# Kernel optimization log

Hardware: AMD Instinct MI355X
Metric: run time of the kernel (lower is better)

## Reference

```python
import jax, jax.numpy as jnp
import numpy as np

C = 256
DR = 32  # C // reduction

def setup_inputs() -> dict:
    key = jax.random.key(0)
    ks = jax.random.split(key, 8)
    B, H, W = 8, 64, 64
    x = jax.random.normal(ks[0], (B, C, H, W), dtype=jnp.float32)
    # 1x1 conv weights stored as [out, in] matrices + biases
    sq = 1.0 / np.sqrt(C)
    Wq = jax.random.uniform(ks[1], (DR, C), minval=-sq, maxval=sq, dtype=jnp.float32)
    bq = jax.random.uniform(ks[2], (DR,), minval=-sq, maxval=sq, dtype=jnp.float32)
    Wk = jax.random.uniform(ks[3], (DR, C), minval=-sq, maxval=sq, dtype=jnp.float32)
    bk = jax.random.uniform(ks[4], (DR,), minval=-sq, maxval=sq, dtype=jnp.float32)
    Wv = jax.random.uniform(ks[5], (C, C), minval=-sq, maxval=sq, dtype=jnp.float32)
    bv = jax.random.uniform(ks[6], (C,), minval=-sq, maxval=sq, dtype=jnp.float32)
    gamma = jnp.zeros((1,), dtype=jnp.float32) + 0.5  # nonzero so output depends on attention
    return {"x": x, "Wq": Wq, "bq": bq, "Wk": Wk, "bk": bk, "Wv": Wv, "bv": bv, "gamma": gamma}

def reference(x, Wq, bq, Wk, bk, Wv, bv, gamma):
    B, Cc, H, W = x.shape
    N = H * W
    xf = x.reshape(B, Cc, N)                                   # [B,C,N]
    q = jnp.einsum('dc,bcn->bdn', Wq, xf) + bq[None, :, None]  # [B,DR,N]
    k = jnp.einsum('dc,bcn->bdn', Wk, xf) + bk[None, :, None]  # [B,DR,N]
    v = jnp.einsum('ec,bcn->ben', Wv, xf) + bv[None, :, None]  # [B,C,N]
    attn = jnp.einsum('bdi,bdj->bij', q, k)                    # [B,N,N]
    attn = jax.nn.softmax(attn, axis=-1)
    out = jnp.einsum('bcj,bij->bci', v, attn)                  # [B,C,N]
    out = out.reshape(B, Cc, H, W)
    return gamma * out + x
```

## Files before the change

### kernel.cpp

```cpp
#include <hip/hip_runtime.h>

#define LOG2E 1.44269504088896340736f

typedef short v8s __attribute__((ext_vector_type(8)));
typedef float v4f __attribute__((ext_vector_type(4)));
typedef unsigned int v2u __attribute__((ext_vector_type(2)));

__device__ __forceinline__ unsigned short f2bf(float f) {
  unsigned int u = __float_as_uint(f);
  u += 0x7fffu + ((u >> 16) & 1u);
  return (unsigned short)(u >> 16);
}

__device__ __forceinline__ unsigned int cvtpk(float lo, float hi) {
  unsigned int r;
  asm("v_cvt_pk_bf16_f32 %0, %1, %2" : "=v"(r) : "v"(lo), "v"(hi));
  return r;
}

#define MFMA16(a, b, c) __builtin_amdgcn_mfma_f32_16x16x32_bf16((a), (b), (c), 0, 0, 0)

static const int CCH = 256, NPIX = 4096;

__global__ void wconv_kernel(const float* __restrict__ Wq, const float* __restrict__ Wk,
                             const float* __restrict__ Wv, unsigned short* __restrict__ wqk,
                             unsigned short* __restrict__ wvb) {
  int idx = blockIdx.x * 256 + threadIdx.x;
  int tot = 64 * 256 + 256 * 256;
  for (int i = idx; i < tot; i += gridDim.x * 256) {
    if (i < 64 * 256) {
      float v = (i < 32 * 256) ? Wq[i] : Wk[i - 32 * 256];
      wqk[i] = f2bf(v);
    } else {
      wvb[i - 64 * 256] = f2bf(Wv[i - 64 * 256]);
    }
  }
}

__global__ void xpose_kernel(const float* __restrict__ x, unsigned short* __restrict__ xT) {
  __shared__ float tile[64][65];
  int bid = blockIdx.x;
  int b = bid >> 8;
  int c0 = ((bid >> 6) & 3) * 64;
  int n0 = (bid & 63) * 64;
  int t = threadIdx.x;
  const float* xp = x + ((size_t)b * CCH + c0) * NPIX + n0;
#pragma unroll
  for (int p = 0; p < 16; ++p) {
    int cc = p * 4 + (t >> 6);
    int nn = t & 63;
    tile[cc][nn] = xp[(size_t)cc * NPIX + nn];
  }
  __syncthreads();
  unsigned short* xo = xT + ((size_t)b * NPIX + n0) * CCH + c0;
#pragma unroll
  for (int p = 0; p < 8; ++p) {
    int nn = p * 8 + (t >> 5);
    int cc = (t & 31) * 2;
    unsigned int pk = (unsigned int)f2bf(tile[cc][nn]) |
                      ((unsigned int)f2bf(tile[cc + 1][nn]) << 16);
    *(unsigned int*)(xo + (size_t)nn * CCH + cc) = pk;
  }
}

__global__ __launch_bounds__(256, 2) void qkproj_kernel(
    const unsigned short* __restrict__ xT, const unsigned short* __restrict__ wqk,
    const float* __restrict__ bq, const float* __restrict__ bk,
    unsigned short* __restrict__ qb, unsigned short* __restrict__ kb) {
  int bid = blockIdx.x;
  int b = bid >> 6;
  int n0 = (bid & 63) * 64;
  int w = threadIdx.x >> 6, lane = threadIdx.x & 63, g = lane >> 4, li = lane & 15;
  int nrow = n0 + 16 * w;
  v4f acc[4];
#pragma unroll
  for (int dt = 0; dt < 4; ++dt) acc[dt] = (v4f){0.f, 0.f, 0.f, 0.f};
#pragma unroll
  for (int ks = 0; ks < 8; ++ks) {
    v8s a = *(const v8s*)(xT + ((size_t)(b * NPIX + nrow + li)) * CCH + ks * 32 + g * 8);
#pragma unroll
    for (int dt = 0; dt < 4; ++dt) {
      v8s bf = *(const v8s*)(wqk + (dt * 16 + li) * 256 + ks * 32 + g * 8);
      acc[dt] = MFMA16(a, bf, acc[dt]);
    }
  }
#pragma unroll
  for (int dt = 0; dt < 4; ++dt) {
    int d = (dt & 1) * 16 + li;
    float bias = (dt < 2) ? bq[d] : bk[d];
    unsigned short* op = (dt < 2) ? qb : kb;
#pragma unroll
    for (int r = 0; r < 4; ++r) {
      int n = nrow + 4 * g + r;
      op[((size_t)(b * NPIX + n)) * 32 + d] = f2bf(acc[dt][r] + bias);
    }
  }
}

__global__ __launch_bounds__(256, 2) void vproj_kernel(
    const unsigned short* __restrict__ xT, const unsigned short* __restrict__ wvb,
    const float* __restrict__ bv, unsigned short* __restrict__ vb) {
  int bid = blockIdx.x;
  int b = bid >> 6;
  int n0 = (bid & 63) * 64;
  int w = threadIdx.x >> 6, lane = threadIdx.x & 63, g = lane >> 4, li = lane & 15;
  v4f acc[4][4];
#pragma unroll
  for (int ct = 0; ct < 4; ++ct)
#pragma unroll
    for (int nt = 0; nt < 4; ++nt) acc[ct][nt] = (v4f){0.f, 0.f, 0.f, 0.f};
#pragma unroll
  for (int ks = 0; ks < 8; ++ks) {
    v8s xf[4];
#pragma unroll
    for (int nt = 0; nt < 4; ++nt)
      xf[nt] = *(const v8s*)(xT + ((size_t)(b * NPIX + n0 + nt * 16 + li)) * CCH + ks * 32 + g * 8);
#pragma unroll
    for (int ct = 0; ct < 4; ++ct) {
      v8s wf = *(const v8s*)(wvb + (w * 64 + ct * 16 + li) * 256 + ks * 32 + g * 8);
#pragma unroll
      for (int nt = 0; nt < 4; ++nt) acc[ct][nt] = MFMA16(wf, xf[nt], acc[ct][nt]);
    }
  }
#pragma unroll
  for (int ct = 0; ct < 4; ++ct)
#pragma unroll
    for (int r = 0; r < 4; ++r) {
      int c = w * 64 + ct * 16 + 4 * g + r;
      float bias = bv[c];
#pragma unroll
      for (int nt = 0; nt < 4; ++nt) {
        int n = n0 + nt * 16 + li;
        vb[((size_t)(b * CCH + c)) * NPIX + n] = f2bf(acc[ct][nt][r] + bias);
      }
    }
}

#define PSWZ(il, jl) (((il) * 64 + (jl)) ^ (((il) & 7) << 3))
__global__ __launch_bounds__(256, 2) void attn_kernel(
    const unsigned short* __restrict__ qb, const unsigned short* __restrict__ kb,
    const unsigned short* __restrict__ vb, const float* __restrict__ x,
    const float* __restrict__ gamma, float* __restrict__ out) {
  __shared__ __align__(16) unsigned short pbuf[2][64 * 64];
  __shared__ float fbuf[2][64];
  __shared__ float lbuf[64];
  int bx = blockIdx.x;
  int wg = (bx & 7) * 64 + (bx >> 3);
  int b = wg >> 6, it = wg & 63;
  int i0 = it * 64;
  int w = threadIdx.x >> 6, lane = threadIdx.x & 63, g = lane >> 4, li = lane & 15;

  v8s qf = *(const v8s*)(qb + ((size_t)(b * NPIX + i0 + w * 16 + li)) * 32 + g * 8);
  float mraw = -1e30f, ml2 = -1.44e30f, ls = 0.f;
  v4f acc[4][4];
#pragma unroll
  for (int ct = 0; ct < 4; ++ct)
#pragma unroll
    for (int itl = 0; itl < 4; ++itl) acc[ct][itl] = (v4f){0.f, 0.f, 0.f, 0.f};
  const v4f vzero = {0.f, 0.f, 0.f, 0.f};

  const unsigned short* kbase = kb + ((size_t)b * NPIX + li) * 32 + g * 8;
  const unsigned short* vb0 = vb + ((size_t)(b * CCH + w * 64 + li)) * NPIX + g * 8;
  const unsigned short* vbc[4];
#pragma unroll
  for (int ct = 0; ct < 4; ++ct) vbc[ct] = vb0 + (size_t)ct * 16 * NPIX;

  v8s kf[4];
#pragma unroll
  for (int jt = 0; jt < 4; ++jt) kf[jt] = *(const v8s*)(kbase + (size_t)(jt * 16) * 32);

  for (int jc = 0; jc < 64; ++jc) {
    int j0 = jc * 64, bsel = jc & 1;
    v4f s[4];
#pragma unroll
    for (int jt = 0; jt < 4; ++jt) s[jt] = MFMA16(kf[jt], qf, vzero);
    int jn = (jc < 63) ? j0 + 64 : j0;
#pragma unroll
    for (int jt = 0; jt < 4; ++jt)
      kf[jt] = *(const v8s*)(kbase + (size_t)(jn + jt * 16) * 32);
    v8s vf[4][2];
#pragma unroll
    for (int ct = 0; ct < 4; ++ct)
#pragma unroll
      for (int sl = 0; sl < 2; ++sl)
        vf[ct][sl] = *(const v8s*)(vbc[ct] + j0 + sl * 32);
    float t0 = fmaxf(fmaxf(s[0][0], s[0][1]), fmaxf(s[0][2], s[0][3]));
    float t1 = fmaxf(fmaxf(s[1][0], s[1][1]), fmaxf(s[1][2], s[1][3]));
    float t2 = fmaxf(fmaxf(s[2][0], s[2][1]), fmaxf(s[2][2], s[2][3]));
    float t3 = fmaxf(fmaxf(s[3][0], s[3][1]), fmaxf(s[3][2], s[3][3]));
    float pmax = fmaxf(fmaxf(t0, t1), fmaxf(t2, t3));
    pmax = fmaxf(pmax, __shfl_xor(pmax, 16, 64));
    pmax = fmaxf(pmax, __shfl_xor(pmax, 32, 64));
    bool upd = pmax > mraw + 8.f;
    float nml2 = upd ? pmax * LOG2E : ml2;
    float fsc = __builtin_amdgcn_exp2f(ml2 - nml2);
    if (upd) { mraw = pmax; ml2 = nml2; }
    float p[4][4];
    float rs = 0.f;
#pragma unroll
    for (int jt = 0; jt < 4; ++jt)
#pragma unroll
      for (int r = 0; r < 4; ++r) {
        float pv = __builtin_amdgcn_exp2f(fmaf(s[jt][r], LOG2E, -nml2));
        p[jt][r] = pv;
        rs += pv;
      }
    rs += __shfl_xor(rs, 16, 64);
    rs += __shfl_xor(rs, 32, 64);
    ls = ls * fsc + rs;
    int il = w * 16 + li;
#pragma unroll
    for (int jt = 0; jt < 4; ++jt) {
      v2u pk;
      pk.x = cvtpk(p[jt][0], p[jt][1]);
      pk.y = cvtpk(p[jt][2], p[jt][3]);
      *(v2u*)(&pbuf[bsel][PSWZ(il, jt * 16 + 4 * g)]) = pk;
    }
    if (g == 0) fbuf[bsel][il] = fsc;
    __syncthreads();
    float fv[4];
#pragma unroll
    for (int itl = 0; itl < 4; ++itl) fv[itl] = fbuf[bsel][itl * 16 + li];
    int anyr = (fv[0] != 1.f) | (fv[1] != 1.f) | (fv[2] != 1.f) | (fv[3] != 1.f);
    if (__any(anyr)) {
#pragma unroll
      for (int itl = 0; itl < 4; ++itl)
#pragma unroll
        for (int ct = 0; ct < 4; ++ct) acc[ct][itl] = acc[ct][itl] * fv[itl];
    }
#pragma unroll
    for (int itl = 0; itl < 4; ++itl) {
      v8s pf[2];
#pragma unroll
      for (int sl = 0; sl < 2; ++sl)
        pf[sl] = *(const v8s*)(&pbuf[bsel][PSWZ(itl * 16 + li, sl * 32 + g * 8)]);
#pragma unroll
      for (int ct = 0; ct < 4; ++ct)
#pragma unroll
        for (int sl = 0; sl < 2; ++sl) acc[ct][itl] = MFMA16(vf[ct][sl], pf[sl], acc[ct][itl]);
    }
  }
  if (g == 0) lbuf[w * 16 + li] = ls;
  __syncthreads();
  float gm = gamma[0];
#pragma unroll
  for (int itl = 0; itl < 4; ++itl) {
    float inv = gm / lbuf[itl * 16 + li];
#pragma unroll
    for (int ct = 0; ct < 4; ++ct)
#pragma unroll
      for (int r = 0; r < 4; ++r) {
        int c = w * 64 + ct * 16 + 4 * g + r;
        size_t idx = ((size_t)(b * CCH + c)) * NPIX + i0 + itl * 16 + li;
        out[idx] = acc[ct][itl][r] * inv + x[idx];
      }
  }
}

extern "C" void kernel_launch(void* const* d_in, const int* in_sizes, int n_in,
                              void* d_out, int out_size, void* d_ws, size_t ws_size,
                              hipStream_t stream) {
  const float* x = (const float*)d_in[0];
  const float* Wq = (const float*)d_in[1];
  const float* bq = (const float*)d_in[2];
  const float* Wk = (const float*)d_in[3];
  const float* bk = (const float*)d_in[4];
  const float* Wv = (const float*)d_in[5];
  const float* bv = (const float*)d_in[6];
  const float* gamma = (const float*)d_in[7];
  float* out = (float*)d_out;
  char* ws = (char*)d_ws;
  unsigned short* xT  = (unsigned short*)(ws);
  unsigned short* qb  = (unsigned short*)(ws + 16777216);
  unsigned short* kb  = (unsigned short*)(ws + 18874368);
  unsigned short* vb  = (unsigned short*)(ws + 20971520);
  unsigned short* wqk = (unsigned short*)(ws + 37748736);
  unsigned short* wvb = (unsigned short*)(ws + 37781504);

  wconv_kernel<<<80, 256, 0, stream>>>(Wq, Wk, Wv, wqk, wvb);
  xpose_kernel<<<2048, 256, 0, stream>>>(x, xT);
  qkproj_kernel<<<512, 256, 0, stream>>>(xT, wqk, bq, bk, qb, kb);
  vproj_kernel<<<512, 256, 0, stream>>>(xT, wvb, bv, vb);
  attn_kernel<<<512, 256, 0, stream>>>(qb, kb, vb, x, gamma, out);
}
```

Baseline: 278.3 us.

## Merge prep kernels and restructure attention with per-wave rows and LDS-staged V

The five launches become three. Weight conversion is folded into the transpose kernel, and the Q/K and V projections share one launch. The attention kernel is restructured so each wave owns 16 query rows across all 256 channels and processes 32-key chunks. V tiles are staged into double-buffered LDS with asynchronous global_load_lds, and the per-chunk P exchange through shared memory and the full workgroup syncthreads are replaced by per-wave P buffers plus a raw barrier with a vmcnt wait. This aims to cut launch overhead, redundant V global reads and sync cost, at the price of twice as many loop iterations and more accumulator registers per wave.

```diff
diff --git a/kernel.cpp b/kernel.cpp
--- a/kernel.cpp
+++ b/kernel.cpp
@@ -18,27 +18,34 @@
   return r;
 }
 
+__device__ __forceinline__ void gld16(const void* g, void* l) {
+  __builtin_amdgcn_global_load_lds(
+      (const __attribute__((address_space(1))) unsigned int*)g,
+      (__attribute__((address_space(3))) unsigned int*)l, 16, 0, 0);
+}
+
 #define MFMA16(a, b, c) __builtin_amdgcn_mfma_f32_16x16x32_bf16((a), (b), (c), 0, 0, 0)
 
 static const int CCH = 256, NPIX = 4096;
 
-__global__ void wconv_kernel(const float* __restrict__ Wq, const float* __restrict__ Wk,
-                             const float* __restrict__ Wv, unsigned short* __restrict__ wqk,
+__global__ void prep1_kernel(const float* __restrict__ x, const float* __restrict__ Wq,
+                             const float* __restrict__ Wk, const float* __restrict__ Wv,
+                             unsigned short* __restrict__ xT, unsigned short* __restrict__ wqk,
                              unsigned short* __restrict__ wvb) {
-  int idx = blockIdx.x * 256 + threadIdx.x;
-  int tot = 64 * 256 + 256 * 256;
-  for (int i = idx; i < tot; i += gridDim.x * 256) {
-    if (i < 64 * 256) {
-      float v = (i < 32 * 256) ? Wq[i] : Wk[i - 32 * 256];
-      wqk[i] = f2bf(v);
-    } else {
-      wvb[i - 64 * 256] = f2bf(Wv[i - 64 * 256]);
-    }
-  }
-}
-
-__global__ void xpose_kernel(const float* __restrict__ x, unsigned short* __restrict__ xT) {
   __shared__ float tile[64][65];
+  if (blockIdx.x >= 2048) {
+    int idx = (blockIdx.x - 2048) * 256 + threadIdx.x;
+    int tot = 64 * 256 + 256 * 256;
+    for (int i = idx; i < tot; i += 64 * 256) {
+      if (i < 64 * 256) {
+        float v = (i < 32 * 256) ? Wq[i] : Wk[i - 32 * 256];
+        wqk[i] = f2bf(v);
+      } else {
+        wvb[i - 64 * 256] = f2bf(Wv[i - 64 * 256]);
+      }
+    }
+    return;
+  }
   int bid = blockIdx.x;
   int b = bid >> 8;
   int c0 = ((bid >> 6) & 3) * 64;
@@ -63,198 +70,185 @@
   }
 }
 
-__global__ __launch_bounds__(256, 2) void qkproj_kernel(
+__global__ __launch_bounds__(256, 2) void prep2_kernel(
     const unsigned short* __restrict__ xT, const unsigned short* __restrict__ wqk,
-    const float* __restrict__ bq, const float* __restrict__ bk,
-    unsigned short* __restrict__ qb, unsigned short* __restrict__ kb) {
-  int bid = blockIdx.x;
-  int b = bid >> 6;
-  int n0 = (bid & 63) * 64;
+    const unsigned short* __restrict__ wvb, const float* __restrict__ bq,
+    const float* __restrict__ bk, const float* __restrict__ bv,
+    unsigned short* __restrict__ qb, unsigned short* __restrict__ kb,
+    unsigned short* __restrict__ vb) {
   int w = threadIdx.x >> 6, lane = threadIdx.x & 63, g = lane >> 4, li = lane & 15;
-  int nrow = n0 + 16 * w;
-  v4f acc[4];
-#pragma unroll
-  for (int dt = 0; dt < 4; ++dt) acc[dt] = (v4f){0.f, 0.f, 0.f, 0.f};
-#pragma unroll
-  for (int ks = 0; ks < 8; ++ks) {
-    v8s a = *(const v8s*)(xT + ((size_t)(b * NPIX + nrow + li)) * CCH + ks * 32 + g * 8);
+  if (blockIdx.x < 512) {
+    int bid = blockIdx.x;
+    int b = bid >> 6;
+    int n0 = (bid & 63) * 64;
+    int nrow = n0 + 16 * w;
+    v4f acc[4];
+#pragma unroll
+    for (int dt = 0; dt < 4; ++dt) acc[dt] = (v4f){0.f, 0.f, 0.f, 0.f};
+#pragma unroll
+    for (int ks = 0; ks < 8; ++ks) {
+      v8s a = *(const v8s*)(xT + ((size_t)(b * NPIX + nrow + li)) * CCH + ks * 32 + g * 8);
+#pragma unroll
+      for (int dt = 0; dt < 4; ++dt) {
+        v8s bf = *(const v8s*)(wqk + (dt * 16 + li) * 256 + ks * 32 + g * 8);
+        acc[dt] = MFMA16(a, bf, acc[dt]);
+      }
+    }
 #pragma unroll
     for (int dt = 0; dt < 4; ++dt) {
-      v8s bf = *(const v8s*)(wqk + (dt * 16 + li) * 256 + ks * 32 + g * 8);
-      acc[dt] = MFMA16(a, bf, acc[dt]);
-    }
-  }
-#pragma unroll
-  for (int dt = 0; dt < 4; ++dt) {
-    int d = (dt & 1) * 16 + li;
-    float bias = (dt < 2) ? bq[d] : bk[d];
-    unsigned short* op = (dt < 2) ? qb : kb;
-#pragma unroll
-    for (int r = 0; r < 4; ++r) {
-      int n = nrow + 4 * g + r;
-      op[((size_t)(b * NPIX + n)) * 32 + d] = f2bf(acc[dt][r] + bias);
-    }
-  }
-}
-
-__global__ __launch_bounds__(256, 2) void vproj_kernel(
-    const unsigned short* __restrict__ xT, const unsigned short* __restrict__ wvb,
-    const float* __restrict__ bv, unsigned short* __restrict__ vb) {
-  int bid = blockIdx.x;
-  int b = bid >> 6;
-  int n0 = (bid & 63) * 64;
-  int w = threadIdx.x >> 6, lane = threadIdx.x & 63, g = lane >> 4, li = lane & 15;
-  v4f acc[4][4];
-#pragma unroll
-  for (int ct = 0; ct < 4; ++ct)
-#pragma unroll
-    for (int nt = 0; nt < 4; ++nt) acc[ct][nt] = (v4f){0.f, 0.f, 0.f, 0.f};
-#pragma unroll
-  for (int ks = 0; ks < 8; ++ks) {
-    v8s xf[4];
-#pragma unroll
-    for (int nt = 0; nt < 4; ++nt)
-      xf[nt] = *(const v8s*)(xT + ((size_t)(b * NPIX + n0 + nt * 16 + li)) * CCH + ks * 32 + g * 8);
-#pragma unroll
-    for (int ct = 0; ct < 4; ++ct) {
-      v8s wf = *(const v8s*)(wvb + (w * 64 + ct * 16 + li) * 256 + ks * 32 + g * 8);
-#pragma unroll
-      for (int nt = 0; nt < 4; ++nt) acc[ct][nt] = MFMA16(wf, xf[nt], acc[ct][nt]);
-    }
-  }
-#pragma unroll
-  for (int ct = 0; ct < 4; ++ct)
-#pragma unroll
-    for (int r = 0; r < 4; ++r) {
-      int c = w * 64 + ct * 16 + 4 * g + r;
-      float bias = bv[c];
-#pragma unroll
-      for (int nt = 0; nt < 4; ++nt) {
-        int n = n0 + nt * 16 + li;
-        vb[((size_t)(b * CCH + c)) * NPIX + n] = f2bf(acc[ct][nt][r] + bias);
-      }
-    }
-}
-
-#define PSWZ(il, jl) (((il) * 64 + (jl)) ^ (((il) & 7) << 3))
+      int d = (dt & 1) * 16 + li;
+      float bias = (dt < 2) ? bq[d] : bk[d];
+      unsigned short* op = (dt < 2) ? qb : kb;
+#pragma unroll
+      for (int r = 0; r < 4; ++r) {
+        int n = nrow + 4 * g + r;
+        op[((size_t)(b * NPIX + n)) * 32 + d] = f2bf(acc[dt][r] + bias);
+      }
+    }
+  } else {
+    int bid = blockIdx.x - 512;
+    int b = bid >> 6;
+    int n0 = (bid & 63) * 64;
+    v4f acc[4][4];
+#pragma unroll
+    for (int ct = 0; ct < 4; ++ct)
+#pragma unroll
+      for (int nt = 0; nt < 4; ++nt) acc[ct][nt] = (v4f){0.f, 0.f, 0.f, 0.f};
+#pragma unroll
+    for (int ks = 0; ks < 8; ++ks) {
+      v8s xf[4];
+#pragma unroll
+      for (int nt = 0; nt < 4; ++nt)
+        xf[nt] = *(const v8s*)(xT + ((size_t)(b * NPIX + n0 + nt * 16 + li)) * CCH + ks * 32 + g * 8);
+#pragma unroll
+      for (int ct = 0; ct < 4; ++ct) {
+        v8s wf = *(const v8s*)(wvb + (w * 64 + ct * 16 + li) * 256 + ks * 32 + g * 8);
+#pragma unroll
+        for (int nt = 0; nt < 4; ++nt) acc[ct][nt] = MFMA16(wf, xf[nt], acc[ct][nt]);
+      }
+    }
+#pragma unroll
+    for (int ct = 0; ct < 4; ++ct)
+#pragma unroll
+      for (int r = 0; r < 4; ++r) {
+        int c = w * 64 + ct * 16 + 4 * g + r;
+        float bias = bv[c];
+#pragma unroll
+        for (int nt = 0; nt < 4; ++nt) {
+          int n = n0 + nt * 16 + li;
+          vb[((size_t)(b * CCH + c)) * NPIX + n] = f2bf(acc[ct][nt][r] + bias);
+        }
+      }
+  }
+}
+
 __global__ __launch_bounds__(256, 2) void attn_kernel(
     const unsigned short* __restrict__ qb, const unsigned short* __restrict__ kb,
     const unsigned short* __restrict__ vb, const float* __restrict__ x,
     const float* __restrict__ gamma, float* __restrict__ out) {
-  __shared__ __align__(16) unsigned short pbuf[2][64 * 64];
-  __shared__ float fbuf[2][64];
-  __shared__ float lbuf[64];
+  __shared__ __align__(16) char vlds[2][16384];
+  __shared__ __align__(16) char plds[4][1024];
   int bx = blockIdx.x;
   int wg = (bx & 7) * 64 + (bx >> 3);
   int b = wg >> 6, it = wg & 63;
   int i0 = it * 64;
   int w = threadIdx.x >> 6, lane = threadIdx.x & 63, g = lane >> 4, li = lane & 15;
 
+  int c0 = w * 16 + (lane >> 2);
+  int srccol = ((lane & 3) ^ ((lane >> 3) & 3)) << 4;
+  const char* vsrc = (const char*)vb + (((size_t)(b * CCH + c0) * NPIX) << 1) + srccol;
+  int vread0 = li * 64 + ((g ^ ((li >> 1) & 3)) << 4);
+  int psw = (li & 3) << 4;
+  char* pw = &plds[w][0] + li * 64;
+  int po0 = (8 * g) ^ psw;
+  int po1 = (32 + 8 * g) ^ psw;
+  int prd = (16 * g) ^ psw;
+
+  float mraw = -1e30f, ml2 = -1.44e30f, ls = 0.f;
+  v4f acc[16];
+#pragma unroll
+  for (int ct = 0; ct < 16; ++ct) acc[ct] = (v4f){0.f, 0.f, 0.f, 0.f};
+  const v4f vzero = {0.f, 0.f, 0.f, 0.f};
+
   v8s qf = *(const v8s*)(qb + ((size_t)(b * NPIX + i0 + w * 16 + li)) * 32 + g * 8);
-  float mraw = -1e30f, ml2 = -1.44e30f, ls = 0.f;
-  v4f acc[4][4];
-#pragma unroll
-  for (int ct = 0; ct < 4; ++ct)
-#pragma unroll
-    for (int itl = 0; itl < 4; ++itl) acc[ct][itl] = (v4f){0.f, 0.f, 0.f, 0.f};
-  const v4f vzero = {0.f, 0.f, 0.f, 0.f};
-
-  const unsigned short* kbase = kb + ((size_t)b * NPIX + li) * 32 + g * 8;
-  const unsigned short* vb0 = vb + ((size_t)(b * CCH + w * 64 + li)) * NPIX + g * 8;
-  const unsigned short* vbc[4];
-#pragma unroll
-  for (int ct = 0; ct < 4; ++ct) vbc[ct] = vb0 + (size_t)ct * 16 * NPIX;
-
-  v8s kf[4];
-#pragma unroll
-  for (int jt = 0; jt < 4; ++jt) kf[jt] = *(const v8s*)(kbase + (size_t)(jt * 16) * 32);
-
-  for (int jc = 0; jc < 64; ++jc) {
-    int j0 = jc * 64, bsel = jc & 1;
-    v4f s[4];
-#pragma unroll
-    for (int jt = 0; jt < 4; ++jt) s[jt] = MFMA16(kf[jt], qf, vzero);
-    int jn = (jc < 63) ? j0 + 64 : j0;
-#pragma unroll
-    for (int jt = 0; jt < 4; ++jt)
-      kf[jt] = *(const v8s*)(kbase + (size_t)(jn + jt * 16) * 32);
-    v8s vf[4][2];
-#pragma unroll
-    for (int ct = 0; ct < 4; ++ct)
-#pragma unroll
-      for (int sl = 0; sl < 2; ++sl)
-        vf[ct][sl] = *(const v8s*)(vbc[ct] + j0 + sl * 32);
-    float t0 = fmaxf(fmaxf(s[0][0], s[0][1]), fmaxf(s[0][2], s[0][3]));
-    float t1 = fmaxf(fmaxf(s[1][0], s[1][1]), fmaxf(s[1][2], s[1][3]));
-    float t2 = fmaxf(fmaxf(s[2][0], s[2][1]), fmaxf(s[2][2], s[2][3]));
-    float t3 = fmaxf(fmaxf(s[3][0], s[3][1]), fmaxf(s[3][2], s[3][3]));
-    float pmax = fmaxf(fmaxf(t0, t1), fmaxf(t2, t3));
+  {
+    char* dp = &vlds[0][0] + w * 1024;
+    gld16(vsrc, dp);
+    gld16(vsrc + 524288, dp + 4096);
+    gld16(vsrc + 1048576, dp + 8192);
+    gld16(vsrc + 1572864, dp + 12288);
+  }
+  asm volatile("" ::: "memory");
+  const unsigned short* kbase = kb + ((size_t)(b * NPIX) + li) * 32 + g * 8;
+  v8s kf0 = *(const v8s*)(kbase);
+  v8s kf1 = *(const v8s*)(kbase + 512);
+
+  for (int jc = 0; jc < 128; ++jc) {
+    int bs = jc & 1;
+    asm volatile("s_waitcnt vmcnt(2)" ::: "memory");
+    __builtin_amdgcn_s_barrier();
+    asm volatile("" ::: "memory");
+    v4f s0 = MFMA16(kf0, qf, vzero);
+    v4f s1 = MFMA16(kf1, qf, vzero);
+    float pmax = fmaxf(fmaxf(fmaxf(s0[0], s0[1]), fmaxf(s0[2], s0[3])),
+                       fmaxf(fmaxf(s1[0], s1[1]), fmaxf(s1[2], s1[3])));
     pmax = fmaxf(pmax, __shfl_xor(pmax, 16, 64));
     pmax = fmaxf(pmax, __shfl_xor(pmax, 32, 64));
     bool upd = pmax > mraw + 8.f;
     float nml2 = upd ? pmax * LOG2E : ml2;
     float fsc = __builtin_amdgcn_exp2f(ml2 - nml2);
     if (upd) { mraw = pmax; ml2 = nml2; }
-    float p[4][4];
-    float rs = 0.f;
-#pragma unroll
-    for (int jt = 0; jt < 4; ++jt)
-#pragma unroll
-      for (int r = 0; r < 4; ++r) {
-        float pv = __builtin_amdgcn_exp2f(fmaf(s[jt][r], LOG2E, -nml2));
-        p[jt][r] = pv;
-        rs += pv;
-      }
+    float p00 = __builtin_amdgcn_exp2f(fmaf(s0[0], LOG2E, -nml2));
+    float p01 = __builtin_amdgcn_exp2f(fmaf(s0[1], LOG2E, -nml2));
+    float p02 = __builtin_amdgcn_exp2f(fmaf(s0[2], LOG2E, -nml2));
+    float p03 = __builtin_amdgcn_exp2f(fmaf(s0[3], LOG2E, -nml2));
+    float p10 = __builtin_amdgcn_exp2f(fmaf(s1[0], LOG2E, -nml2));
+    float p11 = __builtin_amdgcn_exp2f(fmaf(s1[1], LOG2E, -nml2));
+    float p12 = __builtin_amdgcn_exp2f(fmaf(s1[2], LOG2E, -nml2));
+    float p13 = __builtin_amdgcn_exp2f(fmaf(s1[3], LOG2E, -nml2));
+    float rs = ((p00 + p01) + (p02 + p03)) + ((p10 + p11) + (p12 + p13));
     rs += __shfl_xor(rs, 16, 64);
     rs += __shfl_xor(rs, 32, 64);
     ls = ls * fsc + rs;
-    int il = w * 16 + li;
-#pragma unroll
-    for (int jt = 0; jt < 4; ++jt) {
-      v2u pk;
-      pk.x = cvtpk(p[jt][0], p[jt][1]);
-      pk.y = cvtpk(p[jt][2], p[jt][3]);
-      *(v2u*)(&pbuf[bsel][PSWZ(il, jt * 16 + 4 * g)]) = pk;
-    }
-    if (g == 0) fbuf[bsel][il] = fsc;
-    __syncthreads();
-    float fv[4];
-#pragma unroll
-    for (int itl = 0; itl < 4; ++itl) fv[itl] = fbuf[bsel][itl * 16 + li];
-    int anyr = (fv[0] != 1.f) | (fv[1] != 1.f) | (fv[2] != 1.f) | (fv[3] != 1.f);
-    if (__any(anyr)) {
-#pragma unroll
-      for (int itl = 0; itl < 4; ++itl)
-#pragma unroll
-        for (int ct = 0; ct < 4; ++ct) acc[ct][itl] = acc[ct][itl] * fv[itl];
-    }
-#pragma unroll
-    for (int itl = 0; itl < 4; ++itl) {
-      v8s pf[2];
-#pragma unroll
-      for (int sl = 0; sl < 2; ++sl)
-        pf[sl] = *(const v8s*)(&pbuf[bsel][PSWZ(itl * 16 + li, sl * 32 + g * 8)]);
-#pragma unroll
-      for (int ct = 0; ct < 4; ++ct)
-#pragma unroll
-        for (int sl = 0; sl < 2; ++sl) acc[ct][itl] = MFMA16(vf[ct][sl], pf[sl], acc[ct][itl]);
-    }
-  }
-  if (g == 0) lbuf[w * 16 + li] = ls;
-  __syncthreads();
-  float gm = gamma[0];
-#pragma unroll
-  for (int itl = 0; itl < 4; ++itl) {
-    float inv = gm / lbuf[itl * 16 + li];
-#pragma unroll
-    for (int ct = 0; ct < 4; ++ct)
-#pragma unroll
-      for (int r = 0; r < 4; ++r) {
-        int c = w * 64 + ct * 16 + 4 * g + r;
-        size_t idx = ((size_t)(b * CCH + c)) * NPIX + i0 + itl * 16 + li;
-        out[idx] = acc[ct][itl][r] * inv + x[idx];
-      }
-  }
+    v2u pa, pb2;
+    pa.x = cvtpk(p00, p01);  pa.y = cvtpk(p02, p03);
+    pb2.x = cvtpk(p10, p11); pb2.y = cvtpk(p12, p13);
+    *(v2u*)(pw + po0) = pa;
+    *(v2u*)(pw + po1) = pb2;
+    if (__any(upd)) {
+#pragma unroll
+      for (int ct = 0; ct < 16; ++ct) acc[ct] = acc[ct] * fsc;
+    }
+    v8s pf = *(const v8s*)(pw + prd);
+    const char* vbase = &vlds[bs][0] + vread0;
+#pragma unroll
+    for (int ct = 0; ct < 16; ++ct) {
+      v8s vf = *(const v8s*)(vbase + ct * 1024);
+      acc[ct] = MFMA16(vf, pf, acc[ct]);
+    }
+    int jn = (jc < 127) ? jc + 1 : 127;
+    {
+      const char* sp = vsrc + (size_t)jn * 64;
+      char* dp = &vlds[bs ^ 1][0] + w * 1024;
+      gld16(sp, dp);
+      gld16(sp + 524288, dp + 4096);
+      gld16(sp + 1048576, dp + 8192);
+      gld16(sp + 1572864, dp + 12288);
+    }
+    asm volatile("" ::: "memory");
+    const unsigned short* kp = kbase + (size_t)(jn * 32) * 32;
+    kf0 = *(const v8s*)(kp);
+    kf1 = *(const v8s*)(kp + 512);
+  }
+  float inv = gamma[0] / ls;
+#pragma unroll
+  for (int ct = 0; ct < 16; ++ct)
+#pragma unroll
+    for (int r = 0; r < 4; ++r) {
+      int c = ct * 16 + 4 * g + r;
+      size_t idx = ((size_t)(b * CCH + c)) * NPIX + i0 + w * 16 + li;
+      out[idx] = acc[ct][r] * inv + x[idx];
+    }
 }
 
 extern "C" void kernel_launch(void* const* d_in, const int* in_sizes, int n_in,
@@ -277,9 +271,7 @@
   unsigned short* wqk = (unsigned short*)(ws + 37748736);
   unsigned short* wvb = (unsigned short*)(ws + 37781504);
 
-  wconv_kernel<<<80, 256, 0, stream>>>(Wq, Wk, Wv, wqk, wvb);
-  xpose_kernel<<<2048, 256, 0, stream>>>(x, xT);
-  qkproj_kernel<<<512, 256, 0, stream>>>(xT, wqk, bq, bk, qb, kb);
-  vproj_kernel<<<512, 256, 0, stream>>>(xT, wvb, bv, vb);
+  prep1_kernel<<<2112, 256, 0, stream>>>(x, Wq, Wk, Wv, xT, wqk, wvb);
+  prep2_kernel<<<1024, 256, 0, stream>>>(xT, wqk, wvb, bq, bk, bv, qb, kb, vb);
   attn_kernel<<<512, 256, 0, stream>>>(qb, kb, vb, x, gamma, out);
 }
```

After: 294.5 us. 5.8% more time.
